# Performance work log

Measured on AMD Instinct MI355X. Metric: run time of the kernel, lower is better.

The kernel has to match this reference:

```python
import jax, jax.numpy as jnp
import numpy as np

H, D = 16, 64  # n_heads, head_dim


def l2norm(t):
    # F.normalize(t, p=2, dim=-1)
    return t / jnp.maximum(jnp.linalg.norm(t, axis=-1, keepdims=True), 1e-12)


def setup_inputs() -> dict:
    key = jax.random.key(0)
    ks = jax.random.split(key, 6)
    B, N, C = 2, 2048, 1024
    x = jax.random.normal(ks[0], (B, N, C), jnp.float32)
    pos_bias = jax.random.normal(ks[1], (1, H, N, N), jnp.float32)
    mask = jnp.zeros((B, 1, 1, N), bool)  # attn_mask: True = masked
    Wqkv = jax.random.normal(ks[2], (C, 3 * H * D), jnp.float32) / np.sqrt(C)
    Wout = jax.random.normal(ks[3], (H * D, C), jnp.float32) / np.sqrt(H * D)
    Wpre = jax.random.normal(ks[4], (H, H), jnp.float32) / np.sqrt(H)   # 1x1 conv pre
    bpre = jnp.zeros((H,), jnp.float32)
    Wpost = jax.random.normal(ks[5], (H, H), jnp.float32) / np.sqrt(H)  # 1x1 conv post
    bpost = jnp.zeros((H,), jnp.float32)
    temperature = jnp.float32(15.5)
    return {"x": x, "pos_bias": pos_bias, "mask": mask, "Wqkv": Wqkv,
            "Wout": Wout, "Wpre": Wpre, "bpre": bpre, "Wpost": Wpost,
            "bpost": bpost, "temperature": temperature}


def reference(x, pos_bias, mask, Wqkv, Wout, Wpre, bpre, Wpost, bpost, temperature):
    B, N, C = x.shape
    # qkv: 'b n (h d qkv) -> qkv b h n d'
    qkv = (x @ Wqkv).reshape(B, N, H, D, 3)
    q = jnp.transpose(qkv[..., 0], (0, 2, 1, 3))  # [B,H,N,D]
    k = jnp.transpose(qkv[..., 1], (0, 2, 1, 3))
    v = jnp.transpose(qkv[..., 2], (0, 2, 1, 3))
    q, k = l2norm(q), l2norm(k)  # cosine_sim
    kv = jnp.stack([k, v], axis=0)  # attach_cache with cache=None
    # temperature-scaled cosine-sim scores
    dots = jnp.einsum('bhid,bhjd->bhij', q, k) * temperature
    # talking heads pre (1x1 conv over head channel)
    dots = jnp.einsum('gh,bhij->bgij', Wpre, dots) + bpre[None, :, None, None]
    dots = dots + pos_bias
    dots = jnp.where(mask, -jnp.finfo(dots.dtype).max, dots)
    attn = jax.nn.softmax(dots, axis=-1)
    # talking heads post
    attn = jnp.einsum('gh,bhij->bgij', Wpost, attn) + bpost[None, :, None, None]
    out = jnp.einsum('bhij,bhjd->bhid', attn, v)  # [B,H,N,D]
    out = jnp.transpose(out, (0, 2, 1, 3)).reshape(B, N, H * D) @ Wout
    return (out, kv)
```

## Files before the change

### kernel.cpp

```cpp
#include <hip/hip_runtime.h>
#include <stdint.h>

typedef __attribute__((ext_vector_type(8))) short bf16x8;
typedef __attribute__((ext_vector_type(4))) float f32x4;
typedef __attribute__((ext_vector_type(4))) short short4v;

#define DEV __device__ __forceinline__
#define L2E 1.4426950408889634f

DEV float bf2f(unsigned short s){ union{unsigned int u; float f;} x; x.u = ((unsigned int)s)<<16; return x.f; }
DEV unsigned short f2bf(float f){ union{float f; unsigned int u;} x; x.f = f; x.u += 0x7fffu + ((x.u>>16)&1u); return (unsigned short)(x.u>>16); }

DEV f32x4 mfma16(bf16x8 a, bf16x8 b, f32x4 c){
  return __builtin_amdgcn_mfma_f32_16x16x32_bf16(a, b, c, 0, 0, 0);
}
DEV f32x4 zero4(){ f32x4 z; z[0]=0.f; z[1]=0.f; z[2]=0.f; z[3]=0.f; return z; }
DEV bf16x8 zerob(){ bf16x8 z; z[0]=0;z[1]=0;z[2]=0;z[3]=0;z[4]=0;z[5]=0;z[6]=0;z[7]=0; return z; }
DEV float fexp2(float x){ float r; asm volatile("v_exp_f32 %0, %1" : "=v"(r) : "v"(x)); return r; }
DEV void barw(){ asm volatile("s_waitcnt lgkmcnt(0)" ::: "memory"); __builtin_amdgcn_s_barrier(); }

__global__ __launch_bounds__(256) void k_f32_to_bf16(const float* __restrict__ in, unsigned short* __restrict__ out, int n4){
  int i = blockIdx.x*256 + threadIdx.x;
  if (i < n4){
    float4 v = ((const float4*)in)[i];
    short4v o; o.x=(short)f2bf(v.x); o.y=(short)f2bf(v.y); o.z=(short)f2bf(v.z); o.w=(short)f2bf(v.w);
    ((short4v*)out)[i] = o;
  }
}

__global__ __launch_bounds__(256) void k_convT(const float* __restrict__ in, unsigned short* __restrict__ out, int R, int Cc){
  __shared__ float t[32][33];
  int c0 = blockIdx.x*32, r0 = blockIdx.y*32;
  int tid = threadIdx.x;
  int row = tid>>3, col4 = (tid&7)*4;
  float4 v = *(const float4*)&in[(size_t)(r0+row)*Cc + c0 + col4];
  t[row][col4+0]=v.x; t[row][col4+1]=v.y; t[row][col4+2]=v.z; t[row][col4+3]=v.w;
  __syncthreads();
  short4v o;
  o.x=(short)f2bf(t[col4+0][row]); o.y=(short)f2bf(t[col4+1][row]);
  o.z=(short)f2bf(t[col4+2][row]); o.w=(short)f2bf(t[col4+3][row]);
  *(short4v*)&out[(size_t)(c0+row)*R + r0 + col4] = o;
}

__global__ __launch_bounds__(256) void k_prep(const float* __restrict__ wpre, const float* __restrict__ wpost,
                                              const float* __restrict__ temp,
                                              unsigned short* __restrict__ wpre_t,
                                              unsigned short* __restrict__ wpre_t2,
                                              unsigned short* __restrict__ wpost_b){
  int t = threadIdx.x;
  float T = temp[0];
  wpre_t[t]  = f2bf(wpre[t]*T);
  wpre_t2[t] = f2bf(wpre[t]*T*L2E);
  wpost_b[t] = f2bf(wpost[t]);
}

__global__ __launch_bounds__(256) void k_maskf(const unsigned char* __restrict__ mask, float* __restrict__ maskf){
  int i = blockIdx.x*256 + threadIdx.x;
  if (i < 4096) maskf[i] = mask[i] ? -1e30f : 0.f;
}

template<int OUTF>
__global__ __launch_bounds__(256,2) void k_gemm(const unsigned short* __restrict__ A, const unsigned short* __restrict__ Bt,
                                                void* __restrict__ Cv, int M, int Nn, int K){
  __shared__ unsigned short As[128][72];
  __shared__ unsigned short Bs[128][72];
  int tid = threadIdx.x;
  int n0 = blockIdx.x*128, m0 = blockIdx.y*128;
  int w = tid>>6, lane = tid&63, lg = lane>>4, lp = lane&15;
  int wm = (w>>1)*64, wn = (w&1)*64;
  f32x4 acc[4][4];
  #pragma unroll
  for (int i=0;i<4;++i)
    #pragma unroll
    for (int j=0;j<4;++j) acc[i][j] = zero4();

  for (int kt=0; kt<K; kt+=64){
    #pragma unroll
    for (int cch=0; cch<4; ++cch){
      int e = tid + cch*256; int r = e>>3, cl = (e&7)*8;
      *(bf16x8*)&As[r][cl] = *(const bf16x8*)&A[(size_t)(m0+r)*K + kt + cl];
      *(bf16x8*)&Bs[r][cl] = *(const bf16x8*)&Bt[(size_t)(n0+r)*K + kt + cl];
    }
    __syncthreads();
    #pragma unroll
    for (int ks=0; ks<2; ++ks){
      bf16x8 a[4], b[4];
      #pragma unroll
      for (int mi=0; mi<4; ++mi) a[mi] = *(const bf16x8*)&As[wm+mi*16+lp][ks*32 + lg*8];
      #pragma unroll
      for (int ni=0; ni<4; ++ni) b[ni] = *(const bf16x8*)&Bs[wn+ni*16+lp][ks*32 + lg*8];
      #pragma unroll
      for (int mi=0; mi<4; ++mi)
        #pragma unroll
        for (int ni=0; ni<4; ++ni)
          acc[mi][ni] = mfma16(a[mi], b[ni], acc[mi][ni]);
    }
    __syncthreads();
  }
  #pragma unroll
  for (int mi=0; mi<4; ++mi)
    #pragma unroll
    for (int ni=0; ni<4; ++ni)
      #pragma unroll
      for (int r=0; r<4; ++r){
        int row = m0+wm+mi*16+lg*4+r, col = n0+wn+ni*16+lp;
        if (OUTF) ((float*)Cv)[(size_t)row*Nn+col] = acc[mi][ni][r];
        else ((unsigned short*)Cv)[(size_t)row*Nn+col] = f2bf(acc[mi][ni][r]);
      }
}

__global__ __launch_bounds__(256) void k_split_norm(const unsigned short* __restrict__ qkv,
                                                    unsigned short* __restrict__ q, unsigned short* __restrict__ k,
                                                    unsigned short* __restrict__ v, float* __restrict__ kv_out){
  int w = threadIdx.x>>6, lane = threadIdx.x&63;
  int widx = blockIdx.x*4 + w;
  int h = widx & 15; int bn = widx >> 4;
  int b = bn >> 11; int n = bn & 2047;
  size_t base = (size_t)bn*3072 + h*192 + lane*3;
  float qv = bf2f(qkv[base]), kvv = bf2f(qkv[base+1]), vv = bf2f(qkv[base+2]);
  float nq = qv*qv, nk = kvv*kvv;
  #pragma unroll
  for (int m=1; m<64; m<<=1){ nq += __shfl_xor(nq, m); nk += __shfl_xor(nk, m); }
  float qn = qv / fmaxf(sqrtf(nq), 1e-12f);
  float kn = kvv / fmaxf(sqrtf(nk), 1e-12f);
  size_t idx = ((size_t)(b*16+h)*2048 + n)*64 + lane;
  q[idx] = f2bf(qn); k[idx] = f2bf(kn); v[idx] = f2bf(vv);
  kv_out[idx] = kn;
  kv_out[4194304 + idx] = vv;
}

__global__ __launch_bounds__(256) void k_transpose_v(const unsigned short* __restrict__ v, unsigned short* __restrict__ vt){
  __shared__ unsigned short t[64][72];
  int bh = blockIdx.y; int n0 = blockIdx.x*64;
  int tid = threadIdx.x;
  #pragma unroll
  for (int cch=0; cch<2; ++cch){
    int e = tid + cch*256; int r = e>>3, c8 = (e&7)*8;
    *(bf16x8*)&t[r][c8] = *(const bf16x8*)&v[((size_t)bh*2048 + n0 + r)*64 + c8];
  }
  __syncthreads();
  #pragma unroll
  for (int cch=0; cch<2; ++cch){
    int e = tid + cch*256; int d = e>>3, nn8 = (e&7)*8;
    bf16x8 o;
    #pragma unroll
    for (int i=0;i<8;++i) o[i] = (short)t[nn8+i][d];
    *(bf16x8*)&vt[((size_t)bh*64 + d)*2048 + n0 + nn8] = o;
  }
}

__global__ __launch_bounds__(256) void k_vsum(const unsigned short* __restrict__ v, float* __restrict__ vsum){
  int bg = blockIdx.x;
  int d = threadIdx.x & 63, part = threadIdx.x>>6;
  float s = 0.f;
  for (int n = part*512; n < part*512+512; ++n) s += bf2f(v[((size_t)bg*2048 + n)*64 + d]);
  __shared__ float red[4][64];
  red[part][d] = s; __syncthreads();
  if (part==0) vsum[bg*64 + d] = red[0][d]+red[1][d]+red[2][d]+red[3][d];
}

__global__ __launch_bounds__(512,4) void k_score(
    const unsigned short* __restrict__ q,
    const unsigned short* __restrict__ kk,
    const float* __restrict__ pos_bias,
    const float* __restrict__ maskf,
    const unsigned short* __restrict__ wpre_t2,
    const float* __restrict__ bpre,
    unsigned short* __restrict__ Pb,
    float* __restrict__ part_l)
{
  __shared__ __align__(16) char smem[36864];
  const int tid = threadIdx.x;
  const int w = tid>>6, lane = tid&63, lg = lane>>4, lp = lane&15;
  const int bid = blockIdx.x;
  const int qd = bid>>4, r2 = bid&15;
  const int b = r2>>3, n = qd*8 + (r2&7);
  const int it = n>>2, js = n&3;
  const int i0 = it*16, jsb = js*512;

  *(f32x4*)(smem + tid*72 + 32) = zero4();
  *(f32x4*)(smem + tid*72 + 48) = zero4();

  bf16x8 qf[2][2];
  #pragma unroll
  for (int hh=0; hh<2; ++hh){
    const unsigned short* qb = q + ((size_t)(b*16+2*w+hh)*2048 + i0 + lp)*64;
    qf[hh][0] = *(const bf16x8*)(qb + lg*8);
    qf[hh][1] = *(const bf16x8*)(qb + 32 + lg*8);
  }
  bf16x8 preA = zerob();
  if (lg < 2) preA = *(const bf16x8*)&wpre_t2[lp*16 + lg*8];
  float bpre_s[4];
  #pragma unroll
  for (int r=0;r<4;++r) bpre_s[r] = bpre[lg*4+r]*L2E - 32.0f;

  float sacc[2][4];
  #pragma unroll
  for (int ii=0;ii<2;++ii)
    #pragma unroll
    for (int r=0;r<4;++r) sacc[ii][r] = 0.f;

  const size_t kbase0 = (size_t)(b*16 + 2*w)*131072;
  const size_t kbase1 = (size_t)(b*16 + 2*w+1)*131072;

  bf16x8 k0v[4], k1v[4];
  #pragma unroll
  for (int kf=0; kf<2; ++kf)
    #pragma unroll
    for (int jf=0; jf<2; ++jf){
      size_t off = (size_t)(jsb + jf*16 + lp)*64 + kf*32 + lg*8;
      k0v[kf*2+jf] = *(const bf16x8*)(kk + kbase0 + off);
      k1v[kf*2+jf] = *(const bf16x8*)(kk + kbase1 + off);
    }
  __syncthreads();

  for (int t=0; t<16; ++t){
    const int j0 = jsb + t*32;
    const int j0n = jsb + ((t+1)&15)*32;
    float pbt[4][4];
    #pragma unroll
    for (int cc=0; cc<4; ++cc){
      int il = 2*w + (cc>>1);
      int jl = (cc&1)*16 + lp;
      #pragma unroll
      for (int r=0;r<4;++r)
        pbt[cc][r] = pos_bias[(size_t)(lg*4+r)*4194304 + (size_t)(i0+il)*2048 + j0 + jl];
    }
    float mk0 = maskf[b*2048 + j0 + lp];
    float mk1 = maskf[b*2048 + j0 + 16 + lp];

    f32x4 s0[2], s1[2];
    #pragma unroll
    for (int jf=0;jf<2;++jf){ s0[jf]=zero4(); s1[jf]=zero4(); }
    #pragma unroll
    for (int kf=0; kf<2; ++kf)
      #pragma unroll
      for (int jf=0; jf<2; ++jf){
        s0[jf] = mfma16(qf[0][kf], k0v[kf*2+jf], s0[jf]);
        s1[jf] = mfma16(qf[1][kf], k1v[kf*2+jf], s1[jf]);
      }
    #pragma unroll
    for (int kf=0; kf<2; ++kf)
      #pragma unroll
      for (int jf=0; jf<2; ++jf){
        size_t off = (size_t)(j0n + jf*16 + lp)*64 + kf*32 + lg*8;
        k0v[kf*2+jf] = *(const bf16x8*)(kk + kbase0 + off);
        k1v[kf*2+jf] = *(const bf16x8*)(kk + kbase1 + off);
      }
    #pragma unroll
    for (int jf=0;jf<2;++jf)
      #pragma unroll
      for (int r=0;r<4;++r){
        int ij = (lg*4+r)*32 + jf*16 + lp;
        unsigned int pk = (unsigned int)f2bf(s0[jf][r]) | ((unsigned int)f2bf(s1[jf][r])<<16);
        *(unsigned int*)(smem + ij*72 + w*4) = pk;
      }
    barw();

    #pragma unroll
    for (int cc=0; cc<4; ++cc){
      int c = w*4+cc;
      int il = 2*w + (cc>>1);
      int jl = (cc&1)*16 + lp;
      bf16x8 sfrag = *(const bf16x8*)(smem + (c*16+lp)*72 + lg*16);
      f32x4 pa = mfma16(preA, sfrag, zero4());
      float mkj = (cc&1) ? mk1 : mk0;
      short4v p4;
      float pv[4];
      #pragma unroll
      for (int r=0;r<4;++r){
        float e = fmaf(pbt[cc][r], L2E, pa[r] + bpre_s[r] + mkj);
        pv[r] = fexp2(e);
        sacc[cc>>1][r] += pv[r];
      }
      p4.x = (short)f2bf(pv[0]); p4.y = (short)f2bf(pv[1]);
      p4.z = (short)f2bf(pv[2]); p4.w = (short)f2bf(pv[3]);
      *(short4v*)&Pb[(((size_t)(b*2048 + i0+il)*2048) + j0 + jl)*16 + lg*4] = p4;
    }
    barw();
  }

  #pragma unroll
  for (int ii=0;ii<2;++ii)
    #pragma unroll
    for (int r=0;r<4;++r){
      float v = sacc[ii][r];
      #pragma unroll
      for (int m=1; m<16; m<<=1) v += __shfl_xor(v, m);
      sacc[ii][r] = v;
    }
  if (lp == 0){
    int base = ((b*128+it)*4 + js)*256;
    #pragma unroll
    for (int ii=0;ii<2;++ii){
      float4 st; st.x = sacc[ii][0]; st.y = sacc[ii][1]; st.z = sacc[ii][2]; st.w = sacc[ii][3];
      *(float4*)&part_l[base + (2*w+ii)*16 + lg*4] = st;
    }
  }
}

__global__ __launch_bounds__(512,4) void k_mix(
    const unsigned short* __restrict__ Pb,
    const unsigned short* __restrict__ vt,
    const unsigned short* __restrict__ wpost_b,
    const float* __restrict__ bpost,
    const float* __restrict__ vsum,
    const float* __restrict__ part_l,
    float* __restrict__ pout0,
    float* __restrict__ pout1)
{
  __shared__ __align__(16) char smem[17408];
  float* linv = (float*)(smem + 16384);
  const int tid = threadIdx.x;
  const int w = tid>>6, lane = tid&63, lg = lane>>4, lp = lane&15;
  const int bid = blockIdx.x;
  const int qd = bid>>4, r2 = bid&15;
  const int b = r2>>3, n = qd*8 + (r2&7);
  const int it = n>>1, js = n&1;
  const int i0 = it*16, jsb = js*1024;

  if (tid < 256){
    int base = ((b*128+it)*4)*256 + tid;
    float sum = part_l[base] + part_l[base+256] + part_l[base+512] + part_l[base+768];
    linv[tid] = 1.f/sum;
  }
  __syncthreads();

  bf16x8 postB[2];
  #pragma unroll
  for (int ii=0;ii<2;++ii){
    postB[ii] = zerob();
    if (lg < 2){
      bf16x8 wf = *(const bf16x8*)&wpost_b[lp*16 + lg*8];
      int i = 2*w+ii;
      #pragma unroll
      for (int e=0;e<8;++e){
        float vsc = bf2f((unsigned short)wf[e]) * linv[i*16 + lg*8 + e];
        postB[ii][e] = (short)f2bf(vsc);
      }
    }
  }

  f32x4 oacc[2][4];
  #pragma unroll
  for (int hh=0; hh<2; ++hh)
    #pragma unroll
    for (int df=0; df<4; ++df) oacc[hh][df] = zero4();

  for (int t=0; t<32; ++t){
    const int j0 = jsb + t*32;
    #pragma unroll
    for (int cc=0; cc<4; ++cc){
      int il = 2*w + (cc>>1);
      bf16x8 afr = zerob();
      if (lg < 2)
        afr = *(const bf16x8*)&Pb[(((size_t)(b*2048 + i0+il)*2048) + j0 + (cc&1)*16 + lp)*16 + lg*8];
      f32x4 aa = mfma16(afr, postB[cc>>1], zero4());
      short4v av;
      av.x = (short)f2bf(aa[0]); av.y = (short)f2bf(aa[1]);
      av.z = (short)f2bf(aa[2]); av.w = (short)f2bf(aa[3]);
      int row = lp*16 + il;
      int chunk = ((cc&1)*4 + lg) ^ ((lp ^ il)&6);
      *(short4v*)(smem + row*64 + chunk*8) = av;
    }
    barw();
    #pragma unroll
    for (int hh=0; hh<2; ++hh){
      int gg = 2*w+hh;
      int rrow = gg*16+lp;
      bf16x8 af = *(const bf16x8*)(smem + rrow*64 + (((lg*2) ^ ((gg^lp)&6))*8));
      #pragma unroll
      for (int df=0; df<4; ++df){
        bf16x8 vf = *(const bf16x8*)(vt + ((size_t)(b*16+gg)*64 + df*16 + lp)*2048 + j0 + lg*8);
        oacc[hh][df] = mfma16(af, vf, oacc[hh][df]);
      }
    }
    barw();
  }

  float* po = js ? pout1 : pout0;
  #pragma unroll
  for (int hh=0; hh<2; ++hh){
    int gg = 2*w+hh;
    float bp = (js==0) ? bpost[gg] : 0.f;
    #pragma unroll
    for (int df=0; df<4; ++df){
      int d = df*16+lp;
      float vs = vsum[(b*16+gg)*64 + d];
      #pragma unroll
      for (int r=0;r<4;++r){
        po[((size_t)b*2048 + i0 + lg*4 + r)*1024 + gg*64 + d] = oacc[hh][df][r] + bp*vs;
      }
    }
  }
}

__global__ __launch_bounds__(256) void k_combine(const float* __restrict__ p0, const float* __restrict__ p1,
                                                 unsigned short* __restrict__ ao){
  int i = blockIdx.x*256 + threadIdx.x;
  float4 a = ((const float4*)p0)[i];
  float4 c = ((const float4*)p1)[i];
  short4v o;
  o.x=(short)f2bf(a.x+c.x); o.y=(short)f2bf(a.y+c.y);
  o.z=(short)f2bf(a.z+c.z); o.w=(short)f2bf(a.w+c.w);
  ((short4v*)ao)[i] = o;
}

__global__ __launch_bounds__(512,6) void k_pass1f(
    const unsigned short* __restrict__ q,
    const unsigned short* __restrict__ kk,
    const float* __restrict__ pos_bias,
    const unsigned char* __restrict__ mask,
    const unsigned short* __restrict__ wpre_t,
    const float* __restrict__ bpre,
    float* __restrict__ part_m,
    float* __restrict__ part_l)
{
  __shared__ __align__(16) char smem[40960];
  const int tid = threadIdx.x;
  const int w = tid>>6, lane = tid&63, lg = lane>>4, lp = lane&15;
  const int bid = blockIdx.x;
  const int js = bid & 3, b = (bid>>2)&1, it = bid>>3;
  const int i0 = it*16, jsb = js*512;

  *(f32x4*)(smem + tid*80 + 32) = zero4();
  *(f32x4*)(smem + tid*80 + 48) = zero4();

  bf16x8 qf[2][2];
  #pragma unroll
  for (int hh=0; hh<2; ++hh){
    const unsigned short* qb = q + ((size_t)(b*16+2*w+hh)*2048 + i0 + lp)*64;
    qf[hh][0] = *(const bf16x8*)(qb + lg*8);
    qf[hh][1] = *(const bf16x8*)(qb + 32 + lg*8);
  }
  bf16x8 preB = zerob();
  if (lg < 2) preB = *(const bf16x8*)&wpre_t[lp*16 + lg*8];
  const float bpre_g = bpre[lp];

  float m[2], s[2];
  m[0] = -3.0e38f; m[1] = -3.0e38f; s[0] = 0.f; s[1] = 0.f;
  const size_t kbase0 = (size_t)(b*16 + 2*w)*131072;
  const size_t kbase1 = (size_t)(b*16 + 2*w+1)*131072;

  __syncthreads();

  for (int t=0; t<16; ++t){
    const int j0 = jsb + t*32;
    f32x4 s0[2], s1[2];
    #pragma unroll
    for (int jf=0;jf<2;++jf){ s0[jf]=zero4(); s1[jf]=zero4(); }
    #pragma unroll
    for (int kf=0; kf<2; ++kf){
      #pragma unroll
      for (int jf=0; jf<2; ++jf){
        size_t off = (size_t)(j0 + jf*16 + lp)*64 + kf*32 + lg*8;
        bf16x8 k0 = *(const bf16x8*)(kk + kbase0 + off);
        bf16x8 k1 = *(const bf16x8*)(kk + kbase1 + off);
        s0[jf] = mfma16(qf[0][kf], k0, s0[jf]);
        s1[jf] = mfma16(qf[1][kf], k1, s1[jf]);
      }
    }
    #pragma unroll
    for (int jf=0;jf<2;++jf)
      #pragma unroll
      for (int r=0;r<4;++r){
        int ij = (lg*4+r)*32 + jf*16 + lp;
        unsigned int pk = (unsigned int)f2bf(s0[jf][r]) | ((unsigned int)f2bf(s1[jf][r])<<16);
        *(unsigned int*)(smem + ij*80 + w*4) = pk;
      }
    __syncthreads();

    unsigned int mku0 = *(const unsigned int*)(mask + b*2048 + j0 + lg*4);
    unsigned int mku1 = *(const unsigned int*)(mask + b*2048 + j0 + 16 + lg*4);
    #pragma unroll
    for (int cc=0; cc<4; ++cc){
      int c = w*4+cc;
      bf16x8 afr = *(const bf16x8*)(smem + (c*16+lp)*80 + lg*16);
      f32x4 pa = mfma16(afr, preB, zero4());
      int il = 2*w + (cc>>1);
      int jl = (cc&1)*16 + lg*4;
      float4 pb = *(const float4*)&pos_bias[((size_t)lp*2048 + (i0+il))*2048 + j0 + jl];
      unsigned int mku = (cc&1) ? mku1 : mku0;
      float va0 = pa[0] + pb.x + bpre_g + (((mku    )&255u) ? -1e30f : 0.f);
      float va1 = pa[1] + pb.y + bpre_g + (((mku>> 8)&255u) ? -1e30f : 0.f);
      float va2 = pa[2] + pb.z + bpre_g + (((mku>>16)&255u) ? -1e30f : 0.f);
      float va3 = pa[3] + pb.w + bpre_g + (((mku>>24)&255u) ? -1e30f : 0.f);
      int ii = cc>>1;
      float vm = fmaxf(fmaxf(va0,va1), fmaxf(va2,va3));
      float nm = fmaxf(m[ii], vm);
      s[ii] = s[ii]*__expf(m[ii]-nm) + __expf(va0-nm)+__expf(va1-nm)+__expf(va2-nm)+__expf(va3-nm);
      m[ii] = nm;
    }
    __syncthreads();
  }

  #pragma unroll
  for (int ii=0; ii<2; ++ii){
    #pragma unroll
    for (int mk_=16; mk_<=32; mk_<<=1){
      float m2 = __shfl_xor(m[ii], mk_);
      float l2 = __shfl_xor(s[ii], mk_);
      float nm = fmaxf(m[ii], m2);
      s[ii] = s[ii]*__expf(m[ii]-nm) + l2*__expf(m2-nm);
      m[ii] = nm;
    }
  }
  if (lg == 0){
    int pidx = ((b*128+it)*4 + js)*256;
    #pragma unroll
    for (int ii=0; ii<2; ++ii){
      part_m[pidx + (2*w+ii)*16 + lp] = m[ii];
      part_l[pidx + (2*w+ii)*16 + lp] = s[ii];
    }
  }
}

__global__ __launch_bounds__(512,4) void k_pass2f(
    const unsigned short* __restrict__ q,
    const unsigned short* __restrict__ kk,
    const unsigned short* __restrict__ vt,
    const float* __restrict__ pos_bias,
    const unsigned char* __restrict__ mask,
    const unsigned short* __restrict__ wpre_t,
    const unsigned short* __restrict__ wpost_b,
    const float* __restrict__ bpre,
    const float* __restrict__ bpost,
    const float* __restrict__ vsum,
    const float* __restrict__ part_m,
    const float* __restrict__ part_l,
    float* __restrict__ pout0,
    float* __restrict__ pout1)
{
  __shared__ __align__(16) char smem[61440];
  unsigned short* Al = (unsigned short*)(smem + 40960);
  const int tid = threadIdx.x;
  const int w = tid>>6, lane = tid&63, lg = lane>>4, lp = lane&15;
  const int bid = blockIdx.x;
  const int js = bid & 1, b = (bid>>1)&1, it = bid>>2;
  const int i0 = it*16, jsb = js*1024;

  *(f32x4*)(smem + tid*80 + 32) = zero4();
  *(f32x4*)(smem + tid*80 + 48) = zero4();

  bf16x8 qf[2][2];
  #pragma unroll
  for (int hh=0; hh<2; ++hh){
    const unsigned short* qb = q + ((size_t)(b*16+2*w+hh)*2048 + i0 + lp)*64;
    qf[hh][0] = *(const bf16x8*)(qb + lg*8);
    qf[hh][1] = *(const bf16x8*)(qb + 32 + lg*8);
  }
  bf16x8 preB = zerob(), postB = zerob();
  if (lg < 2){
    preB  = *(const bf16x8*)&wpre_t[lp*16 + lg*8];
    postB = *(const bf16x8*)&wpost_b[lp*16 + lg*8];
  }
  const float bpre_g = bpre[lp];

  float mC[2], linvC[2];
  {
    float lC[2]; mC[0]=mC[1]=-3.0e38f; lC[0]=lC[1]=0.f;
    int base = ((b*128+it)*4)*256;
    #pragma unroll
    for (int sj=0; sj<4; ++sj){
      #pragma unroll
      for (int ii=0; ii<2; ++ii){
        float mp  = part_m[base + sj*256 + (2*w+ii)*16 + lp];
        float lpv = part_l[base + sj*256 + (2*w+ii)*16 + lp];
        float nm = fmaxf(mC[ii], mp);
        lC[ii] = lC[ii]*__expf(mC[ii]-nm) + lpv*__expf(mp-nm);
        mC[ii] = nm;
      }
    }
    linvC[0] = 1.f/lC[0]; linvC[1] = 1.f/lC[1];
  }

  f32x4 oacc[2][4];
  #pragma unroll
  for (int hh=0; hh<2; ++hh)
    #pragma unroll
    for (int df=0; df<4; ++df) oacc[hh][df] = zero4();

  const size_t kbase0 = (size_t)(b*16 + 2*w)*131072;
  const size_t kbase1 = (size_t)(b*16 + 2*w+1)*131072;

  __syncthreads();

  for (int t=0; t<32; ++t){
    const int j0 = jsb + t*32;
    f32x4 s0[2], s1[2];
    #pragma unroll
    for (int jf=0;jf<2;++jf){ s0[jf]=zero4(); s1[jf]=zero4(); }
    #pragma unroll
    for (int kf=0; kf<2; ++kf){
      #pragma unroll
      for (int jf=0; jf<2; ++jf){
        size_t off = (size_t)(j0 + jf*16 + lp)*64 + kf*32 + lg*8;
        bf16x8 k0 = *(const bf16x8*)(kk + kbase0 + off);
        bf16x8 k1 = *(const bf16x8*)(kk + kbase1 + off);
        s0[jf] = mfma16(qf[0][kf], k0, s0[jf]);
        s1[jf] = mfma16(qf[1][kf], k1, s1[jf]);
      }
    }
    #pragma unroll
    for (int jf=0;jf<2;++jf)
      #pragma unroll
      for (int r=0;r<4;++r){
        int ij = (lg*4+r)*32 + jf*16 + lp;
        unsigned int pk = (unsigned int)f2bf(s0[jf][r]) | ((unsigned int)f2bf(s1[jf][r])<<16);
        *(unsigned int*)(smem + ij*80 + w*4) = pk;
      }
    __syncthreads();

    unsigned int mku0 = *(const unsigned int*)(mask + b*2048 + j0 + lg*4);
    unsigned int mku1 = *(const unsigned int*)(mask + b*2048 + j0 + 16 + lg*4);
    #pragma unroll
    for (int cc=0; cc<4; ++cc){
      int c = w*4+cc;
      bf16x8 afr = *(const bf16x8*)(smem + (c*16+lp)*80 + lg*16);
      f32x4 pa = mfma16(afr, preB, zero4());
      int il = 2*w + (cc>>1);
      int jl = (cc&1)*16 + lg*4;
      float4 pb = *(const float4*)&pos_bias[((size_t)lp*2048 + (i0+il))*2048 + j0 + jl];
      unsigned int mku = (cc&1) ? mku1 : mku0;
      float va0 = pa[0] + pb.x + bpre_g + (((mku    )&255u) ? -1e30f : 0.f);
      float va1 = pa[1] + pb.y + bpre_g + (((mku>> 8)&255u) ? -1e30f : 0.f);
      float va2 = pa[2] + pb.z + bpre_g + (((mku>>16)&255u) ? -1e30f : 0.f);
      float va3 = pa[3] + pb.w + bpre_g + (((mku>>24)&255u) ? -1e30f : 0.f);
      int ii = cc>>1;
      int rowb = (c*16 + lg*4);
      *(unsigned short*)(smem + (rowb+0)*80 + lp*2) = f2bf(__expf(va0-mC[ii])*linvC[ii]);
      *(unsigned short*)(smem + (rowb+1)*80 + lp*2) = f2bf(__expf(va1-mC[ii])*linvC[ii]);
      *(unsigned short*)(smem + (rowb+2)*80 + lp*2) = f2bf(__expf(va2-mC[ii])*linvC[ii]);
      *(unsigned short*)(smem + (rowb+3)*80 + lp*2) = f2bf(__expf(va3-mC[ii])*linvC[ii]);
    }
    __syncthreads();

    #pragma unroll
    for (int cc=0; cc<4; ++cc){
      int c = w*4+cc;
      bf16x8 a2 = *(const bf16x8*)(smem + (c*16+lp)*80 + lg*16);
      f32x4 aa = mfma16(a2, postB, zero4());
      int il = 2*w + (cc>>1);
      int jl = (cc&1)*16 + lg*4;
      short4v av;
      av.x = (short)f2bf(aa[0]); av.y = (short)f2bf(aa[1]);
      av.z = (short)f2bf(aa[2]); av.w = (short)f2bf(aa[3]);
      *(short4v*)(smem + 40960 + (lp*16 + il)*80 + jl*2) = av;
    }
    __syncthreads();

    #pragma unroll
    for (int hh=0; hh<2; ++hh){
      int gg = 2*w+hh;
      bf16x8 af = *(const bf16x8*)(smem + 40960 + (gg*16+lp)*80 + lg*16);
      #pragma unroll
      for (int df=0; df<4; ++df){
        bf16x8 vf = *(const bf16x8*)(vt + ((size_t)(b*16+gg)*64 + df*16 + lp)*2048 + j0 + lg*8);
        oacc[hh][df] = mfma16(af, vf, oacc[hh][df]);
      }
    }
    __syncthreads();
  }

  float* po = js ? pout1 : pout0;
  #pragma unroll
  for (int hh=0; hh<2; ++hh){
    int gg = 2*w+hh;
    float bp = (js==0) ? bpost[gg] : 0.f;
    #pragma unroll
    for (int df=0; df<4; ++df){
      int d = df*16+lp;
      float vs = vsum[(b*16+gg)*64 + d];
      #pragma unroll
      for (int r=0;r<4;++r){
        po[((size_t)b*2048 + i0 + lg*4 + r)*1024 + gg*64 + d] = oacc[hh][df][r] + bp*vs;
      }
    }
  }
}

extern "C" void kernel_launch(void* const* d_in, const int* in_sizes, int n_in,
                              void* d_out, int out_size, void* d_ws, size_t ws_size,
                              hipStream_t stream)
{
  const float* x        = (const float*)d_in[0];
  const float* pos_bias = (const float*)d_in[1];
  const unsigned char* mask = (const unsigned char*)d_in[2];
// ... 55 lines not shown
```

Baseline: 548.3 us.

## Double-buffer LDS and prefetch pos_bias/Pb/V tiles in score and mix kernels

```diff
diff --git a/kernel.cpp b/kernel.cpp
--- a/kernel.cpp
+++ b/kernel.cpp
@@ -169,7 +169,7 @@
     unsigned short* __restrict__ Pb,
     float* __restrict__ part_l)
 {
-  __shared__ __align__(16) char smem[36864];
+  __shared__ __align__(16) char smem[40960];
   const int tid = threadIdx.x;
   const int w = tid>>6, lane = tid&63, lg = lane>>4, lp = lane&15;
   const int bid = blockIdx.x;
@@ -178,9 +178,6 @@
   const int it = n>>2, js = n&3;
   const int i0 = it*16, jsb = js*512;
 
-  *(f32x4*)(smem + tid*72 + 32) = zero4();
-  *(f32x4*)(smem + tid*72 + 48) = zero4();
-
   bf16x8 qf[2][2];
   #pragma unroll
   for (int hh=0; hh<2; ++hh){
@@ -212,73 +209,88 @@
       k0v[kf*2+jf] = *(const bf16x8*)(kk + kbase0 + off);
       k1v[kf*2+jf] = *(const bf16x8*)(kk + kbase1 + off);
     }
-  __syncthreads();
-
-  for (int t=0; t<16; ++t){
-    const int j0 = jsb + t*32;
-    const int j0n = jsb + ((t+1)&15)*32;
-    float pbt[4][4];
-    #pragma unroll
-    for (int cc=0; cc<4; ++cc){
-      int il = 2*w + (cc>>1);
-      int jl = (cc&1)*16 + lp;
-      #pragma unroll
-      for (int r=0;r<4;++r)
-        pbt[cc][r] = pos_bias[(size_t)(lg*4+r)*4194304 + (size_t)(i0+il)*2048 + j0 + jl];
-    }
-    float mk0 = maskf[b*2048 + j0 + lp];
-    float mk1 = maskf[b*2048 + j0 + 16 + lp];
-
-    f32x4 s0[2], s1[2];
-    #pragma unroll
-    for (int jf=0;jf<2;++jf){ s0[jf]=zero4(); s1[jf]=zero4(); }
-    #pragma unroll
-    for (int kf=0; kf<2; ++kf)
-      #pragma unroll
-      for (int jf=0; jf<2; ++jf){
-        s0[jf] = mfma16(qf[0][kf], k0v[kf*2+jf], s0[jf]);
-        s1[jf] = mfma16(qf[1][kf], k1v[kf*2+jf], s1[jf]);
-      }
-    #pragma unroll
-    for (int kf=0; kf<2; ++kf)
-      #pragma unroll
-      for (int jf=0; jf<2; ++jf){
-        size_t off = (size_t)(j0n + jf*16 + lp)*64 + kf*32 + lg*8;
-        k0v[kf*2+jf] = *(const bf16x8*)(kk + kbase0 + off);
-        k1v[kf*2+jf] = *(const bf16x8*)(kk + kbase1 + off);
-      }
-    #pragma unroll
-    for (int jf=0;jf<2;++jf)
-      #pragma unroll
-      for (int r=0;r<4;++r){
-        int ij = (lg*4+r)*32 + jf*16 + lp;
-        unsigned int pk = (unsigned int)f2bf(s0[jf][r]) | ((unsigned int)f2bf(s1[jf][r])<<16);
-        *(unsigned int*)(smem + ij*72 + w*4) = pk;
-      }
-    barw();
-
-    #pragma unroll
-    for (int cc=0; cc<4; ++cc){
-      int c = w*4+cc;
-      int il = 2*w + (cc>>1);
-      int jl = (cc&1)*16 + lp;
-      bf16x8 sfrag = *(const bf16x8*)(smem + (c*16+lp)*72 + lg*16);
-      f32x4 pa = mfma16(preA, sfrag, zero4());
-      float mkj = (cc&1) ? mk1 : mk0;
-      short4v p4;
-      float pv[4];
-      #pragma unroll
-      for (int r=0;r<4;++r){
-        float e = fmaf(pbt[cc][r], L2E, pa[r] + bpre_s[r] + mkj);
-        pv[r] = fexp2(e);
-        sacc[cc>>1][r] += pv[r];
-      }
-      p4.x = (short)f2bf(pv[0]); p4.y = (short)f2bf(pv[1]);
-      p4.z = (short)f2bf(pv[2]); p4.w = (short)f2bf(pv[3]);
-      *(short4v*)&Pb[(((size_t)(b*2048 + i0+il)*2048) + j0 + jl)*16 + lg*4] = p4;
-    }
-    barw();
-  }
+  float pbA[4][4], pbB[4][4];
+  float mkA0, mkA1, mkB0, mkB1;
+  #pragma unroll
+  for (int cc=0; cc<4; ++cc){
+    int il = 2*w + (cc>>1);
+    int jl = (cc&1)*16 + lp;
+    #pragma unroll
+    for (int r=0;r<4;++r)
+      pbA[cc][r] = pos_bias[(size_t)(lg*4+r)*4194304 + (size_t)(i0+il)*2048 + jsb + jl];
+  }
+  mkA0 = maskf[b*2048 + jsb + lp];
+  mkA1 = maskf[b*2048 + jsb + 16 + lp];
+
+#define SCORE_TILE(T, PBC, PBN, MC0, MC1, MN0, MN1) do { \
+    const int j0 = jsb + (T)*32; \
+    const int j0n = jsb + (((T)+1)&15)*32; \
+    char* sbuf = smem + ((T)&1)*20480; \
+    f32x4 s0[2], s1[2]; \
+    _Pragma("unroll") \
+    for (int jf=0;jf<2;++jf){ s0[jf]=zero4(); s1[jf]=zero4(); } \
+    _Pragma("unroll") \
+    for (int kf=0; kf<2; ++kf) \
+      _Pragma("unroll") \
+      for (int jf=0; jf<2; ++jf){ \
+        s0[jf] = mfma16(qf[0][kf], k0v[kf*2+jf], s0[jf]); \
+        s1[jf] = mfma16(qf[1][kf], k1v[kf*2+jf], s1[jf]); \
+      } \
+    _Pragma("unroll") \
+    for (int jf=0;jf<2;++jf) \
+      _Pragma("unroll") \
+      for (int r=0;r<4;++r){ \
+        int ij = (lg*4+r)*32 + jf*16 + lp; \
+        unsigned int pk = (unsigned int)f2bf(s0[jf][r]) | ((unsigned int)f2bf(s1[jf][r])<<16); \
+        *(unsigned int*)(sbuf + ij*40 + w*4) = pk; \
+      } \
+    _Pragma("unroll") \
+    for (int kf=0; kf<2; ++kf) \
+      _Pragma("unroll") \
+      for (int jf=0; jf<2; ++jf){ \
+        size_t off = (size_t)(j0n + jf*16 + lp)*64 + kf*32 + lg*8; \
+        k0v[kf*2+jf] = *(const bf16x8*)(kk + kbase0 + off); \
+        k1v[kf*2+jf] = *(const bf16x8*)(kk + kbase1 + off); \
+      } \
+    barw(); \
+    _Pragma("unroll") \
+    for (int cc=0; cc<4; ++cc){ \
+      int il = 2*w + (cc>>1); \
+      int jl = (cc&1)*16 + lp; \
+      _Pragma("unroll") \
+      for (int r=0;r<4;++r) \
+        PBN[cc][r] = pos_bias[(size_t)(lg*4+r)*4194304 + (size_t)(i0+il)*2048 + j0n + jl]; \
+    } \
+    MN0 = maskf[b*2048 + j0n + lp]; \
+    MN1 = maskf[b*2048 + j0n + 16 + lp]; \
+    _Pragma("unroll") \
+    for (int cc=0; cc<4; ++cc){ \
+      int c = w*4+cc; \
+      int il = 2*w + (cc>>1); \
+      int jl = (cc&1)*16 + lp; \
+      bf16x8 sfrag = zerob(); \
+      if (lg < 2) sfrag = *(const bf16x8*)(sbuf + (c*16+lp)*40 + lg*16); \
+      f32x4 pa = mfma16(preA, sfrag, zero4()); \
+      float mkj = (cc&1) ? MC1 : MC0; \
+      short4v p4; \
+      float pv[4]; \
+      _Pragma("unroll") \
+      for (int r=0;r<4;++r){ \
+        float e = fmaf(PBC[cc][r], L2E, pa[r] + bpre_s[r] + mkj); \
+        pv[r] = fexp2(e); \
+        sacc[cc>>1][r] += pv[r]; \
+      } \
+      p4.x = (short)f2bf(pv[0]); p4.y = (short)f2bf(pv[1]); \
+      p4.z = (short)f2bf(pv[2]); p4.w = (short)f2bf(pv[3]); \
+      *(short4v*)&Pb[(((size_t)(b*2048 + i0+il)*2048) + j0 + jl)*16 + lg*4] = p4; \
+    } \
+  } while(0)
+
+  for (int tt=0; tt<8; ++tt){
+    SCORE_TILE(2*tt,   pbA, pbB, mkA0, mkA1, mkB0, mkB1);
+    SCORE_TILE(2*tt+1, pbB, pbA, mkB0, mkB1, mkA0, mkA1);
+  }
+#undef SCORE_TILE
 
   #pragma unroll
   for (int ii=0;ii<2;++ii)
@@ -309,8 +321,8 @@
     float* __restrict__ pout0,
     float* __restrict__ pout1)
 {
-  __shared__ __align__(16) char smem[17408];
-  float* linv = (float*)(smem + 16384);
+  __shared__ __align__(16) char smem[33792];
+  float* linv = (float*)(smem + 32768);
   const int tid = threadIdx.x;
   const int w = tid>>6, lane = tid&63, lg = lane>>4, lp = lane&15;
   const int bid = blockIdx.x;
@@ -347,36 +359,60 @@
     #pragma unroll
     for (int df=0; df<4; ++df) oacc[hh][df] = zero4();
 
-  for (int t=0; t<32; ++t){
-    const int j0 = jsb + t*32;
-    #pragma unroll
-    for (int cc=0; cc<4; ++cc){
-      int il = 2*w + (cc>>1);
-      bf16x8 afr = zerob();
-      if (lg < 2)
-        afr = *(const bf16x8*)&Pb[(((size_t)(b*2048 + i0+il)*2048) + j0 + (cc&1)*16 + lp)*16 + lg*8];
-      f32x4 aa = mfma16(afr, postB[cc>>1], zero4());
-      short4v av;
-      av.x = (short)f2bf(aa[0]); av.y = (short)f2bf(aa[1]);
-      av.z = (short)f2bf(aa[2]); av.w = (short)f2bf(aa[3]);
-      int row = lp*16 + il;
-      int chunk = ((cc&1)*4 + lg) ^ ((lp ^ il)&6);
-      *(short4v*)(smem + row*64 + chunk*8) = av;
-    }
-    barw();
-    #pragma unroll
-    for (int hh=0; hh<2; ++hh){
-      int gg = 2*w+hh;
-      int rrow = gg*16+lp;
-      bf16x8 af = *(const bf16x8*)(smem + rrow*64 + (((lg*2) ^ ((gg^lp)&6))*8));
-      #pragma unroll
-      for (int df=0; df<4; ++df){
-        bf16x8 vf = *(const bf16x8*)(vt + ((size_t)(b*16+gg)*64 + df*16 + lp)*2048 + j0 + lg*8);
-        oacc[hh][df] = mfma16(af, vf, oacc[hh][df]);
-      }
-    }
-    barw();
-  }
+  bf16x8 pbC[4], pbN[4];
+  #pragma unroll
+  for (int cc=0; cc<4; ++cc){
+    pbC[cc] = zerob();
+    int il = 2*w + (cc>>1);
+    if (lg < 2)
+      pbC[cc] = *(const bf16x8*)&Pb[(((size_t)(b*2048 + i0+il)*2048) + jsb + (cc&1)*16 + lp)*16 + lg*8];
+  }
+
+#define MIX_TILE(T, PC, PN) do { \
+    const int j0 = jsb + (T)*32; \
+    const int j0n = jsb + (((T)+1)&31)*32; \
+    char* abuf = smem + ((T)&1)*16384; \
+    bf16x8 vfr[2][4]; \
+    _Pragma("unroll") \
+    for (int hh=0; hh<2; ++hh) \
+      _Pragma("unroll") \
+      for (int df=0; df<4; ++df) \
+        vfr[hh][df] = *(const bf16x8*)(vt + ((size_t)(b*16+2*w+hh)*64 + df*16 + lp)*2048 + j0 + lg*8); \
+    _Pragma("unroll") \
+    for (int cc=0; cc<4; ++cc){ \
+      int il = 2*w + (cc>>1); \
+      f32x4 aa = mfma16(PC[cc], postB[cc>>1], zero4()); \
+      short4v av; \
+      av.x = (short)f2bf(aa[0]); av.y = (short)f2bf(aa[1]); \
+      av.z = (short)f2bf(aa[2]); av.w = (short)f2bf(aa[3]); \
+      int row = lp*16 + il; \
+      int chunk = ((cc&1)*4 + lg) ^ ((lp ^ il)&6); \
+      *(short4v*)(abuf + row*64 + chunk*8) = av; \
+    } \
+    _Pragma("unroll") \
+    for (int cc=0; cc<4; ++cc){ \
+      int il = 2*w + (cc>>1); \
+      PN[cc] = zerob(); \
+      if (lg < 2) \
+        PN[cc] = *(const bf16x8*)&Pb[(((size_t)(b*2048 + i0+il)*2048) + j0n + (cc&1)*16 + lp)*16 + lg*8]; \
+    } \
+    barw(); \
+    _Pragma("unroll") \
+    for (int hh=0; hh<2; ++hh){ \
+      int gg = 2*w+hh; \
+      int rrow = gg*16+lp; \
+      bf16x8 af = *(const bf16x8*)(abuf + rrow*64 + (((lg*2) ^ ((gg^lp)&6))*8)); \
+      _Pragma("unroll") \
+      for (int df=0; df<4; ++df) \
+        oacc[hh][df] = mfma16(af, vfr[hh][df], oacc[hh][df]); \
+    } \
+  } while(0)
+
+  for (int tt=0; tt<16; ++tt){
+    MIX_TILE(2*tt,   pbC, pbN);
+    MIX_TILE(2*tt+1, pbN, pbC);
+  }
+#undef MIX_TILE
 
   float* po = js ? pout1 : pout0;
   #pragma unroll
@@ -532,7 +568,6 @@
     float* __restrict__ pout1)
 {
   __shared__ __align__(16) char smem[61440];
-  unsigned short* Al = (unsigned short*)(smem + 40960);
   const int tid = threadIdx.x;
   const int w = tid>>6, lane = tid&63, lg = lane>>4, lp = lane&15;
   const int bid = blockIdx.x;
```

Result: slower. 928.9 us (+69.4%).

## Double-buffer LDS and prefetch operands one tile ahead in score and mix kernels

Applied to the files above, without the earlier changes.

```diff
diff --git a/kernel.cpp b/kernel.cpp
--- a/kernel.cpp
+++ b/kernel.cpp
@@ -159,6 +159,77 @@
   if (part==0) vsum[bg*64 + d] = red[0][d]+red[1][d]+red[2][d]+red[3][d];
 }
 
+DEV void score_tile(
+    int j0, int j0n, char* sbuf,
+    const unsigned short* __restrict__ kk, size_t kbase0, size_t kbase1,
+    const float* __restrict__ pos_bias, const float* __restrict__ maskf, int mbase,
+    const bf16x8 (&qf)[2][2], bf16x8 preA, const float (&bpre_s)[4],
+    bf16x8 (&k0v)[4], bf16x8 (&k1v)[4],
+    float (&PBC)[4][4], float (&PBN)[4][4],
+    float (&sacc)[2][4],
+    unsigned short* __restrict__ Pb, int b, int i0,
+    int w, int lg, int lp)
+{
+  #pragma unroll
+  for (int cc=0; cc<4; ++cc){
+    int il = 2*w + (cc>>1);
+    int jl = (cc&1)*16 + lp;
+    #pragma unroll
+    for (int r=0;r<4;++r)
+      PBN[cc][r] = pos_bias[(size_t)(lg*4+r)*4194304 + (size_t)(i0+il)*2048 + j0n + jl];
+  }
+  f32x4 s0[2], s1[2];
+  #pragma unroll
+  for (int jf=0;jf<2;++jf){ s0[jf]=zero4(); s1[jf]=zero4(); }
+  #pragma unroll
+  for (int kf=0; kf<2; ++kf)
+    #pragma unroll
+    for (int jf=0; jf<2; ++jf){
+      s0[jf] = mfma16(qf[0][kf], k0v[kf*2+jf], s0[jf]);
+      s1[jf] = mfma16(qf[1][kf], k1v[kf*2+jf], s1[jf]);
+    }
+  #pragma unroll
+  for (int jf=0;jf<2;++jf)
+    #pragma unroll
+    for (int r=0;r<4;++r){
+      int ij = (lg*4+r)*32 + jf*16 + lp;
+      unsigned int pk = (unsigned int)f2bf(s0[jf][r]) | ((unsigned int)f2bf(s1[jf][r])<<16);
+      int col = w ^ (((ij>>7)&1)<<2);
+      *(unsigned int*)(sbuf + ij*40 + col*4) = pk;
+    }
+  #pragma unroll
+  for (int kf=0; kf<2; ++kf)
+    #pragma unroll
+    for (int jf=0; jf<2; ++jf){
+      size_t off = (size_t)(j0n + jf*16 + lp)*64 + kf*32 + lg*8;
+      k0v[kf*2+jf] = *(const bf16x8*)(kk + kbase0 + off);
+      k1v[kf*2+jf] = *(const bf16x8*)(kk + kbase1 + off);
+    }
+  float mk0 = maskf[mbase + j0 + lp];
+  float mk1 = maskf[mbase + j0 + 16 + lp];
+  barw();
+  #pragma unroll
+  for (int cc=0; cc<4; ++cc){
+    int c = w*4+cc;
+    int il = 2*w + (cc>>1);
+    int jl = (cc&1)*16 + lp;
+    bf16x8 sfrag = zerob();
+    if (lg < 2) sfrag = *(const bf16x8*)(sbuf + (c*16+lp)*40 + ((lg ^ ((c>>3)&1))<<4));
+    f32x4 pa = mfma16(preA, sfrag, zero4());
+    float mkj = (cc&1) ? mk1 : mk0;
+    float pv0 = fexp2(fmaf(PBC[cc][0], L2E, pa[0] + bpre_s[0] + mkj));
+    float pv1 = fexp2(fmaf(PBC[cc][1], L2E, pa[1] + bpre_s[1] + mkj));
+    float pv2 = fexp2(fmaf(PBC[cc][2], L2E, pa[2] + bpre_s[2] + mkj));
+    float pv3 = fexp2(fmaf(PBC[cc][3], L2E, pa[3] + bpre_s[3] + mkj));
+    sacc[cc>>1][0] += pv0; sacc[cc>>1][1] += pv1;
+    sacc[cc>>1][2] += pv2; sacc[cc>>1][3] += pv3;
+    short4v p4;
+    p4.x = (short)f2bf(pv0); p4.y = (short)f2bf(pv1);
+    p4.z = (short)f2bf(pv2); p4.w = (short)f2bf(pv3);
+    *(short4v*)&Pb[(((size_t)(b*2048 + i0+il)*2048) + j0 + jl)*16 + lg*4] = p4;
+  }
+}
+
 __global__ __launch_bounds__(512,4) void k_score(
     const unsigned short* __restrict__ q,
     const unsigned short* __restrict__ kk,
@@ -169,7 +240,7 @@
     unsigned short* __restrict__ Pb,
     float* __restrict__ part_l)
 {
-  __shared__ __align__(16) char smem[36864];
+  __shared__ __align__(16) char smem[40960];
   const int tid = threadIdx.x;
   const int w = tid>>6, lane = tid&63, lg = lane>>4, lp = lane&15;
   const int bid = blockIdx.x;
@@ -177,9 +248,7 @@
   const int b = r2>>3, n = qd*8 + (r2&7);
   const int it = n>>2, js = n&3;
   const int i0 = it*16, jsb = js*512;
-
-  *(f32x4*)(smem + tid*72 + 32) = zero4();
-  *(f32x4*)(smem + tid*72 + 48) = zero4();
+  const int mbase = b*2048;
 
   bf16x8 qf[2][2];
   #pragma unroll
@@ -212,72 +281,24 @@
       k0v[kf*2+jf] = *(const bf16x8*)(kk + kbase0 + off);
       k1v[kf*2+jf] = *(const bf16x8*)(kk + kbase1 + off);
     }
-  __syncthreads();
-
-  for (int t=0; t<16; ++t){
-    const int j0 = jsb + t*32;
-    const int j0n = jsb + ((t+1)&15)*32;
-    float pbt[4][4];
-    #pragma unroll
-    for (int cc=0; cc<4; ++cc){
-      int il = 2*w + (cc>>1);
-      int jl = (cc&1)*16 + lp;
-      #pragma unroll
-      for (int r=0;r<4;++r)
-        pbt[cc][r] = pos_bias[(size_t)(lg*4+r)*4194304 + (size_t)(i0+il)*2048 + j0 + jl];
-    }
-    float mk0 = maskf[b*2048 + j0 + lp];
-    float mk1 = maskf[b*2048 + j0 + 16 + lp];
-
-    f32x4 s0[2], s1[2];
-    #pragma unroll
-    for (int jf=0;jf<2;++jf){ s0[jf]=zero4(); s1[jf]=zero4(); }
-    #pragma unroll
-    for (int kf=0; kf<2; ++kf)
-      #pragma unroll
-      for (int jf=0; jf<2; ++jf){
-        s0[jf] = mfma16(qf[0][kf], k0v[kf*2+jf], s0[jf]);
-        s1[jf] = mfma16(qf[1][kf], k1v[kf*2+jf], s1[jf]);
-      }
-    #pragma unroll
-    for (int kf=0; kf<2; ++kf)
-      #pragma unroll
-      for (int jf=0; jf<2; ++jf){
-        size_t off = (size_t)(j0n + jf*16 + lp)*64 + kf*32 + lg*8;
-        k0v[kf*2+jf] = *(const bf16x8*)(kk + kbase0 + off);
-        k1v[kf*2+jf] = *(const bf16x8*)(kk + kbase1 + off);
-      }
-    #pragma unroll
-    for (int jf=0;jf<2;++jf)
-      #pragma unroll
-      for (int r=0;r<4;++r){
-        int ij = (lg*4+r)*32 + jf*16 + lp;
-        unsigned int pk = (unsigned int)f2bf(s0[jf][r]) | ((unsigned int)f2bf(s1[jf][r])<<16);
-        *(unsigned int*)(smem + ij*72 + w*4) = pk;
-      }
-    barw();
-
-    #pragma unroll
-    for (int cc=0; cc<4; ++cc){
-      int c = w*4+cc;
-      int il = 2*w + (cc>>1);
-      int jl = (cc&1)*16 + lp;
-      bf16x8 sfrag = *(const bf16x8*)(smem + (c*16+lp)*72 + lg*16);
-      f32x4 pa = mfma16(preA, sfrag, zero4());
-      float mkj = (cc&1) ? mk1 : mk0;
-      short4v p4;
-      float pv[4];
-      #pragma unroll
-      for (int r=0;r<4;++r){
-        float e = fmaf(pbt[cc][r], L2E, pa[r] + bpre_s[r] + mkj);
-        pv[r] = fexp2(e);
-        sacc[cc>>1][r] += pv[r];
-      }
-      p4.x = (short)f2bf(pv[0]); p4.y = (short)f2bf(pv[1]);
-      p4.z = (short)f2bf(pv[2]); p4.w = (short)f2bf(pv[3]);
-      *(short4v*)&Pb[(((size_t)(b*2048 + i0+il)*2048) + j0 + jl)*16 + lg*4] = p4;
-    }
-    barw();
+  float pbA[4][4], pbB[4][4];
+  #pragma unroll
+  for (int cc=0; cc<4; ++cc){
+    int il = 2*w + (cc>>1);
+    int jl = (cc&1)*16 + lp;
+    #pragma unroll
+    for (int r=0;r<4;++r)
+      pbA[cc][r] = pos_bias[(size_t)(lg*4+r)*4194304 + (size_t)(i0+il)*2048 + jsb + jl];
+  }
+
+  for (int tt=0; tt<8; ++tt){
+    int t0 = 2*tt, t1 = 2*tt+1;
+    score_tile(jsb + t0*32, jsb + ((t0+1)&15)*32, smem + (t0&1)*20480,
+               kk, kbase0, kbase1, pos_bias, maskf, mbase,
+               qf, preA, bpre_s, k0v, k1v, pbA, pbB, sacc, Pb, b, i0, w, lg, lp);
+    score_tile(jsb + t1*32, jsb + ((t1+1)&15)*32, smem + (t1&1)*20480,
+               kk, kbase0, kbase1, pos_bias, maskf, mbase,
+               qf, preA, bpre_s, k0v, k1v, pbB, pbA, sacc, Pb, b, i0, w, lg, lp);
   }
 
   #pragma unroll
@@ -296,6 +317,50 @@
       float4 st; st.x = sacc[ii][0]; st.y = sacc[ii][1]; st.z = sacc[ii][2]; st.w = sacc[ii][3];
       *(float4*)&part_l[base + (2*w+ii)*16 + lg*4] = st;
     }
+  }
+}
+
+DEV void mix_tile(
+    int j0, int j0n, char* abuf,
+    const unsigned short* __restrict__ Pb,
+    const unsigned short* __restrict__ vt,
+    const bf16x8 (&postB)[2],
+    bf16x8 (&PC)[4], bf16x8 (&PN)[4],
+    f32x4 (&oacc)[2][4],
+    int b, int i0, int w, int lg, int lp)
+{
+  #pragma unroll
+  for (int cc=0; cc<4; ++cc){
+    int il = 2*w + (cc>>1);
+    PN[cc] = zerob();
+    if (lg < 2)
+      PN[cc] = *(const bf16x8*)&Pb[(((size_t)(b*2048 + i0+il)*2048) + j0n + (cc&1)*16 + lp)*16 + lg*8];
+  }
+  bf16x8 vfr[2][4];
+  #pragma unroll
+  for (int hh=0; hh<2; ++hh)
+    #pragma unroll
+    for (int df=0; df<4; ++df)
+      vfr[hh][df] = *(const bf16x8*)(vt + ((size_t)(b*16+2*w+hh)*64 + df*16 + lp)*2048 + j0 + lg*8);
+  #pragma unroll
+  for (int cc=0; cc<4; ++cc){
+    int il = 2*w + (cc>>1);
+    f32x4 aa = mfma16(PC[cc], postB[cc>>1], zero4());
+    short4v av;
+    av.x = (short)f2bf(aa[0]); av.y = (short)f2bf(aa[1]);
+    av.z = (short)f2bf(aa[2]); av.w = (short)f2bf(aa[3]);
+    int row = lp*16 + il;
+    int chunk = ((cc&1)*4 + lg) ^ ((lp ^ il)&6);
+    *(short4v*)(abuf + row*64 + chunk*8) = av;
+  }
+  barw();
+  #pragma unroll
+  for (int hh=0; hh<2; ++hh){
+    int gg = 2*w+hh;
+    bf16x8 af = *(const bf16x8*)(abuf + (gg*16+lp)*64 + (((lg*2) ^ ((gg^lp)&6))*8));
+    #pragma unroll
+    for (int df=0; df<4; ++df)
+      oacc[hh][df] = mfma16(af, vfr[hh][df], oacc[hh][df]);
   }
 }
 
@@ -309,8 +374,8 @@
     float* __restrict__ pout0,
     float* __restrict__ pout1)
 {
-  __shared__ __align__(16) char smem[17408];
-  float* linv = (float*)(smem + 16384);
+  __shared__ __align__(16) char smem[33792];
+  float* linv = (float*)(smem + 32768);
   const int tid = threadIdx.x;
   const int w = tid>>6, lane = tid&63, lg = lane>>4, lp = lane&15;
   const int bid = blockIdx.x;
@@ -347,35 +412,22 @@
     #pragma unroll
     for (int df=0; df<4; ++df) oacc[hh][df] = zero4();
 
-  for (int t=0; t<32; ++t){
-    const int j0 = jsb + t*32;
-    #pragma unroll
-    for (int cc=0; cc<4; ++cc){
-      int il = 2*w + (cc>>1);
-      bf16x8 afr = zerob();
-      if (lg < 2)
-        afr = *(const bf16x8*)&Pb[(((size_t)(b*2048 + i0+il)*2048) + j0 + (cc&1)*16 + lp)*16 + lg*8];
-      f32x4 aa = mfma16(afr, postB[cc>>1], zero4());
-      short4v av;
-      av.x = (short)f2bf(aa[0]); av.y = (short)f2bf(aa[1]);
-      av.z = (short)f2bf(aa[2]); av.w = (short)f2bf(aa[3]);
-      int row = lp*16 + il;
-      int chunk = ((cc&1)*4 + lg) ^ ((lp ^ il)&6);
-      *(short4v*)(smem + row*64 + chunk*8) = av;
-    }
-    barw();
-    #pragma unroll
-    for (int hh=0; hh<2; ++hh){
-      int gg = 2*w+hh;
-      int rrow = gg*16+lp;
-      bf16x8 af = *(const bf16x8*)(smem + rrow*64 + (((lg*2) ^ ((gg^lp)&6))*8));
-      #pragma unroll
-      for (int df=0; df<4; ++df){
-        bf16x8 vf = *(const bf16x8*)(vt + ((size_t)(b*16+gg)*64 + df*16 + lp)*2048 + j0 + lg*8);
-        oacc[hh][df] = mfma16(af, vf, oacc[hh][df]);
-      }
-    }
-    barw();
+  bf16x8 pbC[4], pbN[4];
+  #pragma unroll
+  for (int cc=0; cc<4; ++cc){
+    pbC[cc] = zerob();
+    int il = 2*w + (cc>>1);
+    if (lg < 2)
+      pbC[cc] = *(const bf16x8*)&Pb[(((size_t)(b*2048 + i0+il)*2048) + jsb + (cc&1)*16 + lp)*16 + lg*8];
+  }
+  __syncthreads();
+
+  for (int tt=0; tt<16; ++tt){
+    int t0 = 2*tt, t1 = 2*tt+1;
+    mix_tile(jsb + t0*32, jsb + ((t0+1)&31)*32, smem + (t0&1)*16384,
+             Pb, vt, postB, pbC, pbN, oacc, b, i0, w, lg, lp);
+    mix_tile(jsb + t1*32, jsb + ((t1+1)&31)*32, smem + (t1&1)*16384,
+             Pb, vt, postB, pbN, pbC, oacc, b, i0, w, lg, lp);
   }
 
   float* po = js ? pout1 : pout0;
@@ -532,7 +584,6 @@
     float* __restrict__ pout1)
 {
   __shared__ __align__(16) char smem[61440];
-  unsigned short* Al = (unsigned short*)(smem + 40960);
   const int tid = threadIdx.x;
   const int w = tid>>6, lane = tid&63, lg = lane>>4, lp = lane&15;
   const int bid = blockIdx.x;
```

New measurement: 862.7 us. +57.3%, slower.

## Double-buffer LDS in score and mix kernels to drop one barrier per tile

Applied to the files above, without the earlier changes.

```diff
diff --git a/kernel.cpp b/kernel.cpp
--- a/kernel.cpp
+++ b/kernel.cpp
@@ -169,7 +169,7 @@
     unsigned short* __restrict__ Pb,
     float* __restrict__ part_l)
 {
-  __shared__ __align__(16) char smem[36864];
+  __shared__ __align__(16) char smem[40960];
   const int tid = threadIdx.x;
   const int w = tid>>6, lane = tid&63, lg = lane>>4, lp = lane&15;
   const int bid = blockIdx.x;
@@ -178,9 +178,6 @@
   const int it = n>>2, js = n&3;
   const int i0 = it*16, jsb = js*512;
 
-  *(f32x4*)(smem + tid*72 + 32) = zero4();
-  *(f32x4*)(smem + tid*72 + 48) = zero4();
-
   bf16x8 qf[2][2];
   #pragma unroll
   for (int hh=0; hh<2; ++hh){
@@ -212,11 +209,11 @@
       k0v[kf*2+jf] = *(const bf16x8*)(kk + kbase0 + off);
       k1v[kf*2+jf] = *(const bf16x8*)(kk + kbase1 + off);
     }
-  __syncthreads();
 
   for (int t=0; t<16; ++t){
     const int j0 = jsb + t*32;
     const int j0n = jsb + ((t+1)&15)*32;
+    char* sbuf = smem + (t&1)*20480;
     float pbt[4][4];
     #pragma unroll
     for (int cc=0; cc<4; ++cc){
@@ -238,6 +235,14 @@
       for (int jf=0; jf<2; ++jf){
         s0[jf] = mfma16(qf[0][kf], k0v[kf*2+jf], s0[jf]);
         s1[jf] = mfma16(qf[1][kf], k1v[kf*2+jf], s1[jf]);
+      }
+    #pragma unroll
+    for (int jf=0;jf<2;++jf)
+      #pragma unroll
+      for (int r=0;r<4;++r){
+        int ij = (lg*4+r)*32 + jf*16 + lp;
+        unsigned int pk = (unsigned int)f2bf(s0[jf][r]) | ((unsigned int)f2bf(s1[jf][r])<<16);
+        *(unsigned int*)(sbuf + ij*40 + w*4) = pk;
       }
     #pragma unroll
     for (int kf=0; kf<2; ++kf)
@@ -247,14 +252,6 @@
         k0v[kf*2+jf] = *(const bf16x8*)(kk + kbase0 + off);
         k1v[kf*2+jf] = *(const bf16x8*)(kk + kbase1 + off);
       }
-    #pragma unroll
-    for (int jf=0;jf<2;++jf)
-      #pragma unroll
-      for (int r=0;r<4;++r){
-        int ij = (lg*4+r)*32 + jf*16 + lp;
-        unsigned int pk = (unsigned int)f2bf(s0[jf][r]) | ((unsigned int)f2bf(s1[jf][r])<<16);
-        *(unsigned int*)(smem + ij*72 + w*4) = pk;
-      }
     barw();
 
     #pragma unroll
@@ -262,22 +259,21 @@
       int c = w*4+cc;
       int il = 2*w + (cc>>1);
       int jl = (cc&1)*16 + lp;
-      bf16x8 sfrag = *(const bf16x8*)(smem + (c*16+lp)*72 + lg*16);
+      bf16x8 sfrag = zerob();
+      if (lg < 2) sfrag = *(const bf16x8*)(sbuf + (c*16+lp)*40 + lg*16);
       f32x4 pa = mfma16(preA, sfrag, zero4());
       float mkj = (cc&1) ? mk1 : mk0;
+      float pv0 = fexp2(fmaf(pbt[cc][0], L2E, pa[0] + bpre_s[0] + mkj));
+      float pv1 = fexp2(fmaf(pbt[cc][1], L2E, pa[1] + bpre_s[1] + mkj));
+      float pv2 = fexp2(fmaf(pbt[cc][2], L2E, pa[2] + bpre_s[2] + mkj));
+      float pv3 = fexp2(fmaf(pbt[cc][3], L2E, pa[3] + bpre_s[3] + mkj));
+      sacc[cc>>1][0] += pv0; sacc[cc>>1][1] += pv1;
+      sacc[cc>>1][2] += pv2; sacc[cc>>1][3] += pv3;
       short4v p4;
-      float pv[4];
-      #pragma unroll
-      for (int r=0;r<4;++r){
-        float e = fmaf(pbt[cc][r], L2E, pa[r] + bpre_s[r] + mkj);
-        pv[r] = fexp2(e);
-        sacc[cc>>1][r] += pv[r];
-      }
-      p4.x = (short)f2bf(pv[0]); p4.y = (short)f2bf(pv[1]);
-      p4.z = (short)f2bf(pv[2]); p4.w = (short)f2bf(pv[3]);
+      p4.x = (short)f2bf(pv0); p4.y = (short)f2bf(pv1);
+      p4.z = (short)f2bf(pv2); p4.w = (short)f2bf(pv3);
       *(short4v*)&Pb[(((size_t)(b*2048 + i0+il)*2048) + j0 + jl)*16 + lg*4] = p4;
     }
-    barw();
   }
 
   #pragma unroll
@@ -309,8 +305,8 @@
     float* __restrict__ pout0,
     float* __restrict__ pout1)
 {
-  __shared__ __align__(16) char smem[17408];
-  float* linv = (float*)(smem + 16384);
+  __shared__ __align__(16) char smem[33792];
+  float* linv = (float*)(smem + 32768);
   const int tid = threadIdx.x;
   const int w = tid>>6, lane = tid&63, lg = lane>>4, lp = lane&15;
   const int bid = blockIdx.x;
@@ -347,35 +343,45 @@
     #pragma unroll
     for (int df=0; df<4; ++df) oacc[hh][df] = zero4();
 
+  __syncthreads();
+
   for (int t=0; t<32; ++t){
     const int j0 = jsb + t*32;
+    char* abuf = smem + (t&1)*16384;
+    bf16x8 pfr[4];
     #pragma unroll
     for (int cc=0; cc<4; ++cc){
       int il = 2*w + (cc>>1);
-      bf16x8 afr = zerob();
+      pfr[cc] = zerob();
       if (lg < 2)
-        afr = *(const bf16x8*)&Pb[(((size_t)(b*2048 + i0+il)*2048) + j0 + (cc&1)*16 + lp)*16 + lg*8];
-      f32x4 aa = mfma16(afr, postB[cc>>1], zero4());
+        pfr[cc] = *(const bf16x8*)&Pb[(((size_t)(b*2048 + i0+il)*2048) + j0 + (cc&1)*16 + lp)*16 + lg*8];
+    }
+    bf16x8 vfr[2][4];
+    #pragma unroll
+    for (int hh=0; hh<2; ++hh)
+      #pragma unroll
+      for (int df=0; df<4; ++df)
+        vfr[hh][df] = *(const bf16x8*)(vt + ((size_t)(b*16+2*w+hh)*64 + df*16 + lp)*2048 + j0 + lg*8);
+    #pragma unroll
+    for (int cc=0; cc<4; ++cc){
+      int il = 2*w + (cc>>1);
+      f32x4 aa = mfma16(pfr[cc], postB[cc>>1], zero4());
       short4v av;
       av.x = (short)f2bf(aa[0]); av.y = (short)f2bf(aa[1]);
       av.z = (short)f2bf(aa[2]); av.w = (short)f2bf(aa[3]);
       int row = lp*16 + il;
       int chunk = ((cc&1)*4 + lg) ^ ((lp ^ il)&6);
-      *(short4v*)(smem + row*64 + chunk*8) = av;
+      *(short4v*)(abuf + row*64 + chunk*8) = av;
     }
     barw();
     #pragma unroll
     for (int hh=0; hh<2; ++hh){
       int gg = 2*w+hh;
-      int rrow = gg*16+lp;
-      bf16x8 af = *(const bf16x8*)(smem + rrow*64 + (((lg*2) ^ ((gg^lp)&6))*8));
-      #pragma unroll
-      for (int df=0; df<4; ++df){
-        bf16x8 vf = *(const bf16x8*)(vt + ((size_t)(b*16+gg)*64 + df*16 + lp)*2048 + j0 + lg*8);
-        oacc[hh][df] = mfma16(af, vf, oacc[hh][df]);
-      }
-    }
-    barw();
+      bf16x8 af = *(const bf16x8*)(abuf + (gg*16+lp)*64 + (((lg*2) ^ ((gg^lp)&6))*8));
+      #pragma unroll
+      for (int df=0; df<4; ++df)
+        oacc[hh][df] = mfma16(af, vfr[hh][df], oacc[hh][df]);
+    }
   }
 
   float* po = js ? pout1 : pout0;
@@ -532,7 +538,6 @@
     float* __restrict__ pout1)
 {
   __shared__ __align__(16) char smem[61440];
-  unsigned short* Al = (unsigned short*)(smem + 40960);
   const int tid = threadIdx.x;
   const int w = tid>>6, lane = tid&63, lg = lane>>4, lp = lane&15;
   const int bid = blockIdx.x;
```

Measured after the change: 522.2 us. 4.8% less time.
